# Performance work log

Hardware: AMD Instinct MI355X
Metric: run time of the kernel (lower is better)

## Reference

```python
import jax, jax.numpy as jnp
import numpy as np

B = 8192
G = 8          # num_groups (fixed by hardcoded bias of size 8)
L = 4096       # input_length


def setup_inputs() -> dict:
    key = jax.random.key(0)
    kx, kw, kb = jax.random.split(key, 3)
    x = jax.random.normal(kx, (B, G, L), dtype=jnp.float32)
    # kaiming_normal_ on (1, L, G): fan_in = G (last dim of >2D tensor per torch fan calc
    # uses dim1 as fan_in = L for a (1,L,G) tensor -> std = sqrt(2/L))
    std = np.sqrt(2.0 / L).astype(np.float32)
    weight = jax.random.normal(kw, (1, L, G), dtype=jnp.float32) * std
    bias = jax.random.uniform(kb, (G,), dtype=jnp.float32) - 0.5
    return {"x": x, "weight": weight, "bias": bias}


def reference(x, weight, bias):
    # Original: diagonal(matmul(x, weight) + bias, dim1=1, dim2=2).
    # diag(x @ W)[b, g] = sum_l x[b, g, l] * W[l, g]  -> compute directly,
    # skipping the unused off-diagonal GEMM outputs (same math).
    out = jnp.einsum("bgl,lg->bg", x, weight[0]) + bias  # (B, G)
    return out
```

## Files before the change

kernel.cpp:

```cpp
#include <hip/hip_runtime.h>


constexpr int Bsz = 8192;
constexpr int G   = 8;
constexpr int L   = 4096;

__global__ __launch_bounds__(256) void transpose_w_kernel(const float* __restrict__ w,
                                                          float* __restrict__ wt) {
    int idx = blockIdx.x * 256 + threadIdx.x;
    if (idx < L * G) {
        int l = idx >> 3;
        int g = idx & (G - 1);
        wt[g * L + l] = w[idx];
    }
}

template <bool TRANSPOSED>
__global__ __launch_bounds__(256) void gfc_kernel(const float* __restrict__ x,
                                                  const float* __restrict__ w,
                                                  const float* __restrict__ bias,
                                                  float* __restrict__ out) {
    const int wid  = threadIdx.x >> 6;
    const int lane = threadIdx.x & 63;
    const int row  = blockIdx.x * 4 + wid;
    const int g    = row & (G - 1);

    const float4* __restrict__ xr =
        reinterpret_cast<const float4*>(x) + (size_t)row * (L / 4);

    float acc[4] = {0.f, 0.f, 0.f, 0.f};

    if (TRANSPOSED) {
        const float4* __restrict__ wr =
            reinterpret_cast<const float4*>(w) + (size_t)g * (L / 4);
#pragma unroll
        for (int it = 0; it < 16; ++it) {
            float4 xv = xr[it * 64 + lane];
            float4 wv = wr[it * 64 + lane];
            float a = acc[it & 3];
            a = fmaf(xv.x, wv.x, a);
            a = fmaf(xv.y, wv.y, a);
            a = fmaf(xv.z, wv.z, a);
            a = fmaf(xv.w, wv.w, a);
            acc[it & 3] = a;
        }
    } else {
#pragma unroll
        for (int it = 0; it < 16; ++it) {
            float4 xv = xr[it * 64 + lane];
            int l = (it * 64 + lane) * 4;
            float a = acc[it & 3];
            a = fmaf(xv.x, w[(l + 0) * G + g], a);
            a = fmaf(xv.y, w[(l + 1) * G + g], a);
            a = fmaf(xv.z, w[(l + 2) * G + g], a);
            a = fmaf(xv.w, w[(l + 3) * G + g], a);
            acc[it & 3] = a;
        }
    }

    float acc_s = (acc[0] + acc[1]) + (acc[2] + acc[3]);

#pragma unroll
    for (int off = 32; off > 0; off >>= 1)
        acc_s += __shfl_down(acc_s, off, 64);

    if (lane == 0)
        out[row] = acc_s + bias[g];
}

extern "C" void kernel_launch(void* const* d_in, const int* in_sizes, int n_in,
                              void* d_out, int out_size, void* d_ws, size_t ws_size,
                              hipStream_t stream) {
    const float* x    = (const float*)d_in[0];
    const float* w    = (const float*)d_in[1];
    const float* bias = (const float*)d_in[2];
    float* out        = (float*)d_out;

    const int num_rows   = Bsz * G;
    const int num_blocks = num_rows / 4;

    if (ws_size >= (size_t)(L * G) * sizeof(float)) {
        float* wt = (float*)d_ws;
        transpose_w_kernel<<<(L * G + 255) / 256, 256, 0, stream>>>(w, wt);
        gfc_kernel<true><<<num_blocks, 256, 0, stream>>>(x, wt, bias, out);
    } else {
        gfc_kernel<false><<<num_blocks, 256, 0, stream>>>(x, w, bias, out);
    }
}
```

Baseline: 1.302 ms.

## Persistent waves keep weight row in registers and stream two x rows per iteration

The kernel moves from one wave per row to a fixed grid of 1024 blocks, where each wave owns one group g. The wave loads that group's weight row into registers once and reuses it across many batch rows. It processes two rows per iteration to keep more loads in flight. This removes the repeated weight reloads, at the cost of higher register pressure (64 float4 values per lane) and fewer resident waves for hiding memory latency.

```diff
diff --git a/kernel.cpp b/kernel.cpp
--- a/kernel.cpp
+++ b/kernel.cpp
@@ -4,6 +4,13 @@
 constexpr int Bsz = 8192;
 constexpr int G   = 8;
 constexpr int L   = 4096;
+constexpr int L4  = L / 4;
+constexpr int NF  = L4 / 64;
+
+constexpr int NBLOCKS       = 1024;
+constexpr int WAVES_TOTAL   = NBLOCKS * 4;
+constexpr int WAVES_PER_G   = WAVES_TOTAL / G;
+constexpr int ROWS_PER_WAVE = Bsz / WAVES_PER_G;
 
 __global__ __launch_bounds__(256) void transpose_w_kernel(const float* __restrict__ w,
                                                           float* __restrict__ wt) {
@@ -16,56 +23,87 @@
 }
 
 template <bool TRANSPOSED>
-__global__ __launch_bounds__(256) void gfc_kernel(const float* __restrict__ x,
-                                                  const float* __restrict__ w,
-                                                  const float* __restrict__ bias,
-                                                  float* __restrict__ out) {
+__global__ __launch_bounds__(256, 2) void gfc_kernel(const float* __restrict__ x,
+                                                     const float* __restrict__ w,
+                                                     const float* __restrict__ bias,
+                                                     float* __restrict__ out) {
     const int wid  = threadIdx.x >> 6;
     const int lane = threadIdx.x & 63;
-    const int row  = blockIdx.x * 4 + wid;
-    const int g    = row & (G - 1);
+    const int wave = blockIdx.x * 4 + wid;
+    const int g    = wave & (G - 1);
+    const int wg   = wave >> 3;
 
-    const float4* __restrict__ xr =
-        reinterpret_cast<const float4*>(x) + (size_t)row * (L / 4);
-
-    float acc[4] = {0.f, 0.f, 0.f, 0.f};
-
+    float4 wv[NF];
     if (TRANSPOSED) {
         const float4* __restrict__ wr =
-            reinterpret_cast<const float4*>(w) + (size_t)g * (L / 4);
+            reinterpret_cast<const float4*>(w) + (size_t)g * L4 + lane;
 #pragma unroll
-        for (int it = 0; it < 16; ++it) {
-            float4 xv = xr[it * 64 + lane];
-            float4 wv = wr[it * 64 + lane];
-            float a = acc[it & 3];
-            a = fmaf(xv.x, wv.x, a);
-            a = fmaf(xv.y, wv.y, a);
-            a = fmaf(xv.z, wv.z, a);
-            a = fmaf(xv.w, wv.w, a);
-            acc[it & 3] = a;
-        }
+        for (int it = 0; it < NF; ++it) wv[it] = wr[it * 64];
     } else {
 #pragma unroll
-        for (int it = 0; it < 16; ++it) {
-            float4 xv = xr[it * 64 + lane];
+        for (int it = 0; it < NF; ++it) {
             int l = (it * 64 + lane) * 4;
-            float a = acc[it & 3];
-            a = fmaf(xv.x, w[(l + 0) * G + g], a);
-            a = fmaf(xv.y, w[(l + 1) * G + g], a);
-            a = fmaf(xv.z, w[(l + 2) * G + g], a);
-            a = fmaf(xv.w, w[(l + 3) * G + g], a);
-            acc[it & 3] = a;
+            wv[it].x = w[(l + 0) * G + g];
+            wv[it].y = w[(l + 1) * G + g];
+            wv[it].z = w[(l + 2) * G + g];
+            wv[it].w = w[(l + 3) * G + g];
         }
     }
 
-    float acc_s = (acc[0] + acc[1]) + (acc[2] + acc[3]);
+    const float bg = bias[g];
+    const float4* __restrict__ xbase = reinterpret_cast<const float4*>(x);
+    const int b0 = wg * ROWS_PER_WAVE;
+
+#pragma unroll 1
+    for (int k = 0; k < ROWS_PER_WAVE; k += 2) {
+        const int rowA = (b0 + k)     * G + g;
+        const int rowB = (b0 + k + 1) * G + g;
+        const float4* __restrict__ xa = xbase + (size_t)rowA * L4 + lane;
+        const float4* __restrict__ xb = xbase + (size_t)rowB * L4 + lane;
+
+        float4 va[NF], vb[NF];
+#pragma unroll
+        for (int it = 0; it < NF; ++it) va[it] = xa[it * 64];
+#pragma unroll
+        for (int it = 0; it < NF; ++it) vb[it] = xb[it * 64];
+
+        float accA[4] = {0.f, 0.f, 0.f, 0.f};
+        float accB[4] = {0.f, 0.f, 0.f, 0.f};
+#pragma unroll
+        for (int it = 0; it < NF; ++it) {
+            float4 xv = va[it], wq = wv[it];
+            float t = accA[it & 3];
+            t = fmaf(xv.x, wq.x, t);
+            t = fmaf(xv.y, wq.y, t);
+            t = fmaf(xv.z, wq.z, t);
+            t = fmaf(xv.w, wq.w, t);
+            accA[it & 3] = t;
+        }
+#pragma unroll
+        for (int it = 0; it < NF; ++it) {
+            float4 xv = vb[it], wq = wv[it];
+            float t = accB[it & 3];
+            t = fmaf(xv.x, wq.x, t);
+            t = fmaf(xv.y, wq.y, t);
+            t = fmaf(xv.z, wq.z, t);
+            t = fmaf(xv.w, wq.w, t);
+            accB[it & 3] = t;
+        }
+
+        float sA = (accA[0] + accA[1]) + (accA[2] + accA[3]);
+        float sB = (accB[0] + accB[1]) + (accB[2] + accB[3]);
 
 #pragma unroll
-    for (int off = 32; off > 0; off >>= 1)
-        acc_s += __shfl_down(acc_s, off, 64);
+        for (int off = 32; off > 0; off >>= 1) {
+            sA += __shfl_down(sA, off, 64);
+            sB += __shfl_down(sB, off, 64);
+        }
 
-    if (lane == 0)
-        out[row] = acc_s + bias[g];
+        if (lane == 0) {
+            out[rowA] = sA + bg;
+            out[rowB] = sB + bg;
+        }
+    }
 }
 
 extern "C" void kernel_launch(void* const* d_in, const int* in_sizes, int n_in,
@@ -76,14 +114,11 @@
     const float* bias = (const float*)d_in[2];
     float* out        = (float*)d_out;
 
-    const int num_rows   = Bsz * G;
-    const int num_blocks = num_rows / 4;
-
     if (ws_size >= (size_t)(L * G) * sizeof(float)) {
         float* wt = (float*)d_ws;
         transpose_w_kernel<<<(L * G + 255) / 256, 256, 0, stream>>>(w, wt);
-        gfc_kernel<true><<<num_blocks, 256, 0, stream>>>(x, wt, bias, out);
+        gfc_kernel<true><<<NBLOCKS, 256, 0, stream>>>(x, wt, bias, out);
     } else {
-        gfc_kernel<false><<<num_blocks, 256, 0, stream>>>(x, w, bias, out);
+        gfc_kernel<false><<<NBLOCKS, 256, 0, stream>>>(x, w, bias, out);
     }
 }
```

Result: no change. 1.296 ms (-0.4%).
